# Performance work log

Hardware: AMD Instinct MI355X
Metric: run time of the kernel (lower is better)

Reference implementation:

```python
import jax, jax.numpy as jnp
import numpy as np

N = 100000   # nodes
E = 1600000  # edges (avg degree 16)
D = 128      # input_dim
K = 8        # pe_k
PE = 32      # pe_out_dim
HID = 64     # SignNet hidden
H = 2        # heads
C = 32       # out_channels per head
NEG_SLOPE = 0.2


def setup_inputs() -> dict:
    key = jax.random.key(0)
    ks = jax.random.split(key, 24)
    w = lambda k, shape, s=0.1: jax.random.normal(k, shape, jnp.float32) * s
    return {
        "x": jax.random.normal(ks[0], (N, D), jnp.float32),
        "lap_eigvec": jax.random.normal(ks[1], (N, K), jnp.float32),
        "edge_index": jax.random.randint(ks[2], (2, E), 0, N, jnp.int64),
        # SignNet params: phi (K->HID->HID), rho (HID->PE)
        "phi_w1": w(ks[3], (K, HID)), "phi_b1": jnp.zeros((HID,), jnp.float32),
        "phi_w2": w(ks[4], (HID, HID)), "phi_b2": jnp.zeros((HID,), jnp.float32),
        "rho_w": w(ks[5], (HID, PE)), "rho_b": jnp.zeros((PE,), jnp.float32),
        # GAT layer 0: in = D+PE = 160 -> H*C = 64
        "W0": w(ks[6], (D + PE, H * C)),
        "asrc0": w(ks[7], (H, C)), "adst0": w(ks[8], (H, C)),
        "b0": jnp.zeros((H * C,), jnp.float32),
        # GAT layer 1: in = H*C = 64 -> H*C = 64
        "W1": w(ks[9], (H * C, H * C)),
        "asrc1": w(ks[10], (H, C)), "adst1": w(ks[11], (H, C)),
        "b1": jnp.zeros((H * C,), jnp.float32),
        # final LayerNorm over H*C
        "ln_g": jnp.ones((H * C,), jnp.float32),
        "ln_b": jnp.zeros((H * C,), jnp.float32),
    }


def _gat_layer(x, src, dst, W, a_src, a_dst, b):
    # x: [N, Fin] -> h: [N, H, C]
    h = (x @ W).reshape(x.shape[0], H, C)
    alpha_s = (h * a_src).sum(-1)  # [N, H]
    alpha_d = (h * a_dst).sum(-1)  # [N, H]
    e = jax.nn.leaky_relu(alpha_s[src] + alpha_d[dst], NEG_SLOPE)  # [E, H]
    # softmax over incoming edges per destination node
    e_max = jax.ops.segment_max(e, dst, num_segments=N)  # [N, H]
    e_exp = jnp.exp(e - e_max[dst])
    denom = jax.ops.segment_sum(e_exp, dst, num_segments=N)
    alpha = e_exp / (denom[dst] + 1e-16)  # [E, H]
    msg = h[src] * alpha[:, :, None]      # [E, H, C]
    out = jax.ops.segment_sum(msg, dst, num_segments=N)
    out = out.reshape(x.shape[0], H * C) + b
    return jax.nn.elu(out)


def reference(x, lap_eigvec, edge_index, phi_w1, phi_b1, phi_w2, phi_b2,
              rho_w, rho_b, W0, asrc0, adst0, b0, W1, asrc1, adst1, b1,
              ln_g, ln_b):
    # SignNet: sign-invariant PE  rho(phi(v) + phi(-v))
    def phi(v):
        return jax.nn.relu(jax.nn.relu(v @ phi_w1 + phi_b1) @ phi_w2 + phi_b2)
    pe = (phi(lap_eigvec) + phi(-lap_eigvec)) @ rho_w + rho_b  # [N, PE]
    h = jnp.concatenate([x, pe], axis=-1)  # [N, D+PE]

    src, dst = edge_index[0], edge_index[1]
    h = _gat_layer(h, src, dst, W0, asrc0, adst0, b0)
    h = _gat_layer(h, src, dst, W1, asrc1, adst1, b1)

    # final LayerNorm
    mu = h.mean(-1, keepdims=True)
    var = ((h - mu) ** 2).mean(-1, keepdims=True)
    return (h - mu) * jax.lax.rsqrt(var + 1e-5) * ln_g + ln_b
```

## Files before the change

### kernel.cpp

```cpp
#include <hip/hip_runtime.h>
#include <cstdint>
#include <cstddef>
#include <cstring>

#define TPB 256
#define TILE 8192

typedef float f32x2 __attribute__((ext_vector_type(2)));

__device__ __forceinline__ ushort f2b(float f) {
    union { float f; uint32_t u; } v; v.f = f;
    uint32_t r = (v.u + 0x7FFFu + ((v.u >> 16) & 1u)) >> 16;
    return (ushort)r;
}
__device__ __forceinline__ float b2f(ushort h) {
    union { uint32_t u; float f; } v; v.u = ((uint32_t)h) << 16;
    return v.f;
}
__device__ __forceinline__ float b2f_lo(uint32_t u) {
    union { uint32_t u; float f; } v; v.u = u << 16;
    return v.f;
}
__device__ __forceinline__ float b2f_hi(uint32_t u) {
    union { uint32_t u; float f; } v; v.u = u & 0xFFFF0000u;
    return v.f;
}
__device__ __forceinline__ float f16lo2f(uint32_t u) {
    union { ushort s; _Float16 h; } v; v.s = (ushort)u;
    return (float)v.h;
}
__device__ __forceinline__ uint32_t pack_f16x2(float p0, float p1) {
    auto hp = __builtin_amdgcn_cvt_pkrtz(p0, p1);
    uint32_t pk;
    __builtin_memcpy(&pk, &hp, 4);
    return pk;
}


__global__ __launch_bounds__(TPB) void k_hist(const int* __restrict__ dst, int* __restrict__ hist,
                                              int E, int NB, int NBLK) {
    __shared__ int hc[512];
    const int t = threadIdx.x, blk = blockIdx.x;
    for (int b = t; b < NB; b += TPB) hc[b] = 0;
    __syncthreads();
    const int e0 = blk * TILE;
    for (int i = t; i < TILE; i += TPB) {
        int e = e0 + i;
        if (e < E) atomicAdd(&hc[dst[e] >> 8], 1);
    }
    __syncthreads();
    for (int b = t; b < NB; b += TPB) hist[b * NBLK + blk] = hc[b];
}


__global__ __launch_bounds__(TPB) void k_scan1(const int* __restrict__ a, int* __restrict__ bsum, int total) {
    __shared__ int sh[TPB];
    int base = blockIdx.x * 1024;
    int s = 0;
#pragma unroll
    for (int j = 0; j < 4; ++j) {
        int idx = base + threadIdx.x * 4 + j;
        if (idx < total) s += a[idx];
    }
    sh[threadIdx.x] = s;
    __syncthreads();
    for (int off = 128; off > 0; off >>= 1) {
        if (threadIdx.x < off) sh[threadIdx.x] += sh[threadIdx.x + off];
        __syncthreads();
    }
    if (threadIdx.x == 0) bsum[blockIdx.x] = sh[0];
}

__global__ void k_scan2(int* __restrict__ bsum, int nb) {
    __shared__ int sh[256];
    int t = threadIdx.x;
    int v = (t < nb) ? bsum[t] : 0;
    sh[t] = v;
    __syncthreads();
    for (int off = 1; off < 256; off <<= 1) {
        int u = (t >= off) ? sh[t - off] : 0;
        __syncthreads();
        sh[t] += u;
        __syncthreads();
    }
    if (t < nb) bsum[t] = sh[t] - v;
}

__global__ __launch_bounds__(TPB) void k_scan3(int* __restrict__ a, const int* __restrict__ bsum, int total) {
    __shared__ int sh[TPB];
    int base = blockIdx.x * 1024;
    int v[4];
    int s = 0;
#pragma unroll
    for (int j = 0; j < 4; ++j) {
        int idx = base + threadIdx.x * 4 + j;
        v[j] = (idx < total) ? a[idx] : 0;
        s += v[j];
    }
    sh[threadIdx.x] = s;
    __syncthreads();
    for (int off = 1; off < TPB; off <<= 1) {
        int t = (threadIdx.x >= off) ? sh[threadIdx.x - off] : 0;
        __syncthreads();
        sh[threadIdx.x] += t;
        __syncthreads();
    }
    int pre = bsum[blockIdx.x] + sh[threadIdx.x] - s;
#pragma unroll
    for (int j = 0; j < 4; ++j) {
        int idx = base + threadIdx.x * 4 + j;
        if (idx < total) { a[idx] = pre; pre += v[j]; }
    }
}

__global__ __launch_bounds__(TPB) void k_part(const int* __restrict__ src, const int* __restrict__ dst,
                                              const int* __restrict__ S, int* __restrict__ part,
                                              int E, int NB, int NBLK) {
    __shared__ int hbase[512];
    __shared__ int hcur[512];
    const int t = threadIdx.x, blk = blockIdx.x;
    for (int b = t; b < NB; b += TPB) { hbase[b] = S[b * NBLK + blk]; hcur[b] = 0; }
    __syncthreads();
    const int e0 = blk * TILE;
    for (int i = t; i < TILE; i += TPB) {
        int e = e0 + i;
        if (e < E) {
            int d = dst[e];
            int bu = d >> 8;
            int r = atomicAdd(&hcur[bu], 1);
            part[hbase[bu] + r] = (src[e] << 8) | (d & 255);
        }
    }
}

__global__ __launch_bounds__(TPB) void k_csr(const int* __restrict__ part, const int* __restrict__ S,
                                             int* __restrict__ offs, int* __restrict__ csr,
                                             int E, int N, int NB, int NBLK) {
    __shared__ int cnt[256];
    __shared__ int pre[256];
    const int t = threadIdx.x, b = blockIdx.x;
    const int bstart = S[b * NBLK];
    const int bend = (b + 1 < NB) ? S[(b + 1) * NBLK] : E;
    cnt[t] = 0;
    __syncthreads();
    for (int e = bstart + t; e < bend; e += TPB) atomicAdd(&cnt[part[e] & 255], 1);
    __syncthreads();
    int c = cnt[t];
    pre[t] = c;
    __syncthreads();
    for (int off = 1; off < 256; off <<= 1) {
        int u = (t >= off) ? pre[t - off] : 0;
        __syncthreads();
        pre[t] += u;
        __syncthreads();
    }
    int ex = pre[t] - c;
    int node = b * 256 + t;
    if (node <= N) offs[node] = bstart + ex;
    pre[t] = ex;
    cnt[t] = 0;
    __syncthreads();
    for (int e = bstart + t; e < bend; e += TPB) {
        int pk = part[e];
        int local = pk & 255;
        int r = atomicAdd(&cnt[local], 1);
        csr[bstart + pre[local] + r] = pk >> 8;
    }
}


__global__ __launch_bounds__(TPB) void k_rinit(const float* __restrict__ rho_w, const float* __restrict__ rho_b,
                                               const float* __restrict__ W0, float* __restrict__ R,
                                               float* __restrict__ cvec) {
    const float* Wpe = W0 + 128 * 64;
    int tid = threadIdx.x;
    for (int idx = tid; idx < 64 * 64; idx += TPB) {
        int r = idx >> 6, cc = idx & 63;
        float s = 0.f;
#pragma unroll
        for (int k = 0; k < 32; ++k) s = fmaf(rho_w[r * 32 + k], Wpe[k * 64 + cc], s);
        R[idx] = s;
    }
    if (tid < 64) {
        float s = 0.f;
#pragma unroll
        for (int k = 0; k < 32; ++k) s = fmaf(rho_b[k], Wpe[k * 64 + tid], s);
        cvec[tid] = s;
    }
}


__global__ __launch_bounds__(TPB) void k_sign(const float* __restrict__ eig,
                                              const float* __restrict__ w1, const float* __restrict__ b1,
                                              const float* __restrict__ w2, const float* __restrict__ b2,
                                              ushort* __restrict__ S, int M) {
    __shared__ float eigS[64][9];
    __shared__ float w1s[512];
    __shared__ float b1s[64];
    __shared__ float Ap[64][65];
    __shared__ float Aq[64][65];
    __shared__ float Ws[64][64];
    const int tid = threadIdx.x;
    const int row0 = blockIdx.x * 64;

    for (int i = tid; i < 512; i += TPB) w1s[i] = w1[i];
    if (tid < 64) b1s[tid] = b1[tid];
    for (int i = tid; i < 1024; i += TPB) {
        float4 v = *(const float4*)(w2 + i * 4);
        Ws[0][i * 4 + 0] = v.x; Ws[0][i * 4 + 1] = v.y; Ws[0][i * 4 + 2] = v.z; Ws[0][i * 4 + 3] = v.w;
    }
    {
        int idx = tid * 2;
        int r = idx >> 3, c = idx & 7;
        int row = row0 + r; int rowc = row < M ? row : M - 1;
        float2 v = *(const float2*)(eig + (size_t)rowc * 8 + c);
        eigS[r][c] = v.x; eigS[r][c + 1] = v.y;
    }
    __syncthreads();

    {
        int r = tid >> 2, csub = tid & 3;
        float ev[8];
#pragma unroll
        for (int k = 0; k < 8; ++k) ev[k] = eigS[r][k];
#pragma unroll
        for (int c0 = 0; c0 < 16; ++c0) {
            int c = csub * 16 + c0;
            float t = 0.f;
#pragma unroll
            for (int k = 0; k < 8; ++k) t = fmaf(ev[k], w1s[k * 64 + c], t);
            float bb = b1s[c];
            Ap[c][r] = fmaxf(t + bb, 0.f);
            Aq[c][r] = fmaxf(bb - t, 0.f);
        }
    }
    __syncthreads();

    const int ty = tid >> 4, tx = tid & 15;
    float accp[4][4] = {{0.f}}, accq[4][4] = {{0.f}};
#pragma unroll 8
    for (int kk = 0; kk < 64; ++kk) {
        float ap[4], aq[4], bw[4];
#pragma unroll
        for (int i = 0; i < 4; ++i) { ap[i] = Ap[kk][ty * 4 + i]; aq[i] = Aq[kk][ty * 4 + i]; }
#pragma unroll
        for (int j = 0; j < 4; ++j) bw[j] = Ws[kk][tx * 4 + j];
#pragma unroll
        for (int i = 0; i < 4; ++i)
#pragma unroll
            for (int j = 0; j < 4; ++j) {
                accp[i][j] = fmaf(ap[i], bw[j], accp[i][j]);
                accq[i][j] = fmaf(aq[i], bw[j], accq[i][j]);
            }
    }
#pragma unroll
    for (int i = 0; i < 4; ++i) {
        int row = row0 + ty * 4 + i;
        if (row >= M) continue;
        ushort4 o;
        ushort* op = (ushort*)&o;
#pragma unroll
        for (int j = 0; j < 4; ++j) {
            int col = tx * 4 + j;
            float bb = b2[col];
            float v = fmaxf(accp[i][j] + bb, 0.f) + fmaxf(accq[i][j] + bb, 0.f);
            op[j] = f2b(v);
        }
        *(ushort4*)(S + (size_t)row * 64 + tx * 4) = o;
    }
}


#define BM 64
#define BK 16

__global__ __launch_bounds__(TPB) void k_mm(const float* __restrict__ A1, int K1,
                                            const ushort* __restrict__ A2, int K2,
                                            const float* __restrict__ Wa, const float* __restrict__ Wb,
                                            const float* __restrict__ bias,
                                            const float* __restrict__ a_s, const float* __restrict__ a_d,
                                            float2* __restrict__ as2, float2* __restrict__ ad2,
                                            ushort* __restrict__ out, int M) {
    __shared__ float As[BK][BM + 4];
    __shared__ float Bs[BK][64];
    const int tid = threadIdx.x;
    const int row0 = blockIdx.x * BM;
    const int K = K1 + K2;
    const int ty = tid >> 4, tx = tid & 15;
    float acc[4][4] = {{0.f}};

    for (int k0 = 0; k0 < K; k0 += BK) {
        {
            int r = tid >> 2;
            int cq = (tid & 3) * 4;
            int row = row0 + r;
            int rowc = row < M ? row : M - 1;
            int c = k0 + cq;
            float4 v;
            if (c < K1) {
                v = *(const float4*)(A1 + (size_t)rowc * K1 + c);
            } else {
                const ushort* p = A2 + (size_t)rowc * K2 + (c - K1);
                ushort4 u = *(const ushort4*)p;
                v = make_float4(b2f(u.x), b2f(u.y), b2f(u.z), b2f(u.w));
            }
            As[cq + 0][r] = v.x; As[cq + 1][r] = v.y; As[cq + 2][r] = v.z; As[cq + 3][r] = v.w;
        }
        {
            int rr = tid >> 4;
            int cq2 = (tid & 15) * 4;
            int kk = k0 + rr;
            const float* Wrow = (kk < K1) ? (Wa + (size_t)kk * 64) : (Wb + (size_t)(kk - K1) * 64);
            float4 wv = *(const float4*)(Wrow + cq2);
            Bs[rr][cq2 + 0] = wv.x; Bs[rr][cq2 + 1] = wv.y; Bs[rr][cq2 + 2] = wv.z; Bs[rr][cq2 + 3] = wv.w;
        }
        __syncthreads();
#pragma unroll
        for (int kk = 0; kk < BK; ++kk) {
            float a[4], bw[4];
#pragma unroll
            for (int i = 0; i < 4; ++i) a[i] = As[kk][ty * 4 + i];
#pragma unroll
            for (int j = 0; j < 4; ++j) bw[j] = Bs[kk][tx * 4 + j];
#pragma unroll
            for (int i = 0; i < 4; ++i)
#pragma unroll
                for (int j = 0; j < 4; ++j)
                    acc[i][j] = fmaf(a[i], bw[j], acc[i][j]);
        }
        __syncthreads();
    }

    float s_acc[4] = {0.f, 0.f, 0.f, 0.f}, d_acc[4] = {0.f, 0.f, 0.f, 0.f};
#pragma unroll
    for (int i = 0; i < 4; ++i) {
#pragma unroll
        for (int j = 0; j < 4; ++j) {
            int col = tx * 4 + j;
            float v = acc[i][j];
            if (bias) v += bias[col];
            acc[i][j] = v;
            s_acc[i] = fmaf(v, a_s[col], s_acc[i]);
            d_acc[i] = fmaf(v, a_d[col], d_acc[i]);
        }
    }
#pragma unroll
    for (int m = 1; m <= 4; m <<= 1) {
#pragma unroll
        for (int i = 0; i < 4; ++i) {
            s_acc[i] += __shfl_xor(s_acc[i], m);
            d_acc[i] += __shfl_xor(d_acc[i], m);
        }
    }
    float s_oth[4], d_oth[4];
#pragma unroll
    for (int i = 0; i < 4; ++i) {
        s_oth[i] = __shfl_xor(s_acc[i], 8);
        d_oth[i] = __shfl_xor(d_acc[i], 8);
    }
#pragma unroll
    for (int i = 0; i < 4; ++i) {
        int row = row0 + ty * 4 + i;
        if (row >= M) continue;
        ushort4 o;
        ushort* op = (ushort*)&o;
#pragma unroll
        for (int j = 0; j < 4; ++j) op[j] = f2b(acc[i][j]);
        *(ushort4*)(out + (size_t)row * 64 + tx * 4) = o;
        if (tx == 0) {
            as2[row] = make_float2(s_acc[i], s_oth[i]);
            ad2[row] = make_float2(d_acc[i], d_oth[i]);
        }
    }
}


template <int DO_LN>
__global__ __launch_bounds__(TPB) void k_agg(const int* __restrict__ offs, const int* __restrict__ csr_src,
                                             const ushort* __restrict__ hb,
                                             const float2* __restrict__ as2,
                                             const float2* __restrict__ ad2,
                                             const float* __restrict__ bias,
                                             const float* __restrict__ ln_g,
                                             const float* __restrict__ ln_b,
                                             void* __restrict__ out_v, int M) {
    __shared__ uint2 ep[4][64];
    int w = (blockIdx.x * blockDim.x + threadIdx.x) >> 6;
    int lane = threadIdx.x & 63;
    int wl = threadIdx.x >> 6;
    if (w >= M) return;
    const int sub = lane & 15;
    const int grp = lane >> 4;
    const int c0 = sub * 4;
    const int head = sub >> 3;
    const int hshift = head << 4;

    float2 adv = ad2[w];
    int beg = offs[w], end = offs[w + 1];
    f32x2 acc01 = {0.f, 0.f}, acc23 = {0.f, 0.f};
    float qs = 0.f;

    for (int base = beg; base < end; base += 64) {
        int nk = end - base;
        if (nk > 64) nk = 64;
        int sidx = csr_src[base + (lane < nk ? lane : 0)];
        float2 av = as2[sidx];
        float e0 = av.x + adv.x; e0 = e0 > 0.f ? e0 : 0.2f * e0;
        float e1 = av.y + adv.y; e1 = e1 > 0.f ? e1 : 0.2f * e1;
        float p0 = __expf(e0), p1 = __expf(e1);
        if (lane >= nk) { p0 = 0.f; p1 = 0.f; }
        ep[wl][lane] = make_uint2((uint32_t)sidx, pack_f16x2(p0, p1));

        int j = 0;
        for (; j + 8 <= nk; j += 8) {
            uint2 eA = ep[wl][j + grp];
            uint2 eB = ep[wl][j + 4 + grp];
            uint2 uA = *(const uint2*)(hb + ((uint32_t)eA.x << 6) + c0);
            uint2 uB = *(const uint2*)(hb + ((uint32_t)eB.x << 6) + c0);
            float qA = f16lo2f(eA.y >> hshift);
            float qB = f16lo2f(eB.y >> hshift);
            qs += qA + qB;
            f32x2 hA01 = {b2f_lo(uA.x), b2f_hi(uA.x)};
            f32x2 hA23 = {b2f_lo(uA.y), b2f_hi(uA.y)};
            f32x2 hB01 = {b2f_lo(uB.x), b2f_hi(uB.x)};
            f32x2 hB23 = {b2f_lo(uB.y), b2f_hi(uB.y)};
            acc01 += qA * hA01;
            acc23 += qA * hA23;
            acc01 += qB * hB01;
            acc23 += qB * hB23;
        }
        for (; j < nk; j += 4) {
            int src = j + grp;
            if (src > 63) src = 63;
            uint2 e = ep[wl][src];
            uint2 u = *(const uint2*)(hb + ((uint32_t)e.x << 6) + c0);
            float q = f16lo2f(e.y >> hshift);
            qs += q;
            f32x2 h01 = {b2f_lo(u.x), b2f_hi(u.x)};
            f32x2 h23 = {b2f_lo(u.y), b2f_hi(u.y)};
            acc01 += q * h01;
            acc23 += q * h23;
        }
    }
    float a0 = acc01.x, a1 = acc01.y, a2 = acc23.x, a3 = acc23.y;
    a0 += __shfl_xor(a0, 16); a0 += __shfl_xor(a0, 32);
    a1 += __shfl_xor(a1, 16); a1 += __shfl_xor(a1, 32);
    a2 += __shfl_xor(a2, 16); a2 += __shfl_xor(a2, 32);
    a3 += __shfl_xor(a3, 16); a3 += __shfl_xor(a3, 32);
    qs += __shfl_xor(qs, 16); qs += __shfl_xor(qs, 32);

    float inv = 1.f / (qs + 1e-16f);
    float4 bb = *(const float4*)(bias + c0);
    float o0 = fmaf(a0, inv, bb.x);
    float o1 = fmaf(a1, inv, bb.y);
    float o2 = fmaf(a2, inv, bb.z);
    float o3 = fmaf(a3, inv, bb.w);
    o0 = o0 > 0.f ? o0 : expm1f(o0);
    o1 = o1 > 0.f ? o1 : expm1f(o1);
    o2 = o2 > 0.f ? o2 : expm1f(o2);
    o3 = o3 > 0.f ? o3 : expm1f(o3);

    if (DO_LN) {
        float mu = o0 + o1 + o2 + o3;
#pragma unroll
        for (int m = 1; m <= 8; m <<= 1) mu += __shfl_xor(mu, m);
        mu *= (1.f / 64.f);
        float dv = (o0 - mu) * (o0 - mu) + (o1 - mu) * (o1 - mu)
                 + (o2 - mu) * (o2 - mu) + (o3 - mu) * (o3 - mu);
#pragma unroll
        for (int m = 1; m <= 8; m <<= 1) dv += __shfl_xor(dv, m);
        dv *= (1.f / 64.f);
        float rs = rsqrtf(dv + 1e-5f);
        float4 g = *(const float4*)(ln_g + c0);
        float4 b = *(const float4*)(ln_b + c0);
        o0 = (o0 - mu) * rs * g.x + b.x;
        o1 = (o1 - mu) * rs * g.y + b.y;
        o2 = (o2 - mu) * rs * g.z + b.z;
        o3 = (o3 - mu) * rs * g.w + b.w;
        if (lane < 16) {
            float4* out = (float4*)out_v;
            out[(size_t)w * 16 + sub] = make_float4(o0, o1, o2, o3);
        }
    } else {
        if (lane < 16) {
            uint2 pk2;
            pk2.x = (uint32_t)f2b(o0) | ((uint32_t)f2b(o1) << 16);
            pk2.y = (uint32_t)f2b(o2) | ((uint32_t)f2b(o3) << 16);
            uint2* out = (uint2*)out_v;
            out[(size_t)w * 16 + sub] = pk2;
        }
    }
}


extern "C" void kernel_launch(void* const* d_in, const int* in_sizes, int n_in,
                              void* d_out, int out_size, void* d_ws, size_t ws_size,
                              hipStream_t stream) {
    const float* x      = (const float*)d_in[0];
    const float* eig    = (const float*)d_in[1];
    const int*   ei     = (const int*)d_in[2];
    const float* phi_w1 = (const float*)d_in[3];
    const float* phi_b1 = (const float*)d_in[4];
    const float* phi_w2 = (const float*)d_in[5];
    const float* phi_b2 = (const float*)d_in[6];
    const float* rho_w  = (const float*)d_in[7];
    const float* rho_b  = (const float*)d_in[8];
    const float* W0     = (const float*)d_in[9];
    const float* asrc0  = (const float*)d_in[10];
    const float* adst0  = (const float*)d_in[11];
    const float* b0     = (const float*)d_in[12];
    const float* W1     = (const float*)d_in[13];
    const float* asrc1  = (const float*)d_in[14];
    const float* adst1  = (const float*)d_in[15];
    const float* b1     = (const float*)d_in[16];
    const float* ln_g   = (const float*)d_in[17];
    const float* ln_b   = (const float*)d_in[18];

    const int N = in_sizes[0] / 128;
    const int E = in_sizes[2] / 2;
    const int* esrc = ei;
    const int* edst = ei + E;

    const int NB   = (N >> 8) + 1;
    const int NBLK = (E + TILE - 1) / TILE;

    auto alignup = [](size_t v) { return (v + 255) & ~(size_t)255; };
    char* w = (char*)d_ws;
    int* S      = (int*)w; w += alignup((size_t)NB * NBLK * 4);
    int* bsum   = (int*)w; w += alignup(4096);
    int* part   = (int*)w; w += alignup((size_t)E * 4);
    int* offs   = (int*)w; w += alignup((size_t)(N + 1) * 4);
    int* csr    = (int*)w; w += alignup((size_t)E * 4);
    ushort* Sb  = (ushort*)w; w += alignup((size_t)N * 64 * 2);
    ushort* hb  = (ushort*)w; w += alignup((size_t)N * 64 * 2);
    ushort* g0b = (ushort*)w; w += alignup((size_t)N * 64 * 2);
    float2* as2 = (float2*)w; w += alignup((size_t)N * 8);
    float2* ad2 = (float2*)w; w += alignup((size_t)N * 8);
    float* R    = (float*)w; w += alignup(64 * 64 * 4);
    float* cvec = (float*)w; w += alignup(64 * 4);

    const int tot = NB * NBLK;
    const int nbS = (tot + 1023) / 1024;
    k_hist<<<NBLK, TPB, 0, stream>>>(edst, S, E, NB, NBLK);
    k_scan1<<<nbS, TPB, 0, stream>>>(S, bsum, tot);
    k_scan2<<<1, 256, 0, stream>>>(bsum, nbS);
    k_scan3<<<nbS, TPB, 0, stream>>>(S, bsum, tot);
    k_part<<<NBLK, TPB, 0, stream>>>(esrc, edst, S, part, E, NB, NBLK);
    k_csr<<<NB, TPB, 0, stream>>>(part, S, offs, csr, E, N, NB, NBLK);

    k_rinit<<<1, TPB, 0, stream>>>(rho_w, rho_b, W0, R, cvec);

    int gM = (N + BM - 1) / BM;
    k_sign<<<gM, TPB, 0, stream>>>(eig, phi_w1, phi_b1, phi_w2, phi_b2, Sb, N);

    k_mm<<<gM, TPB, 0, stream>>>(x, 128, Sb, 64, W0, R, cvec, asrc0, adst0, as2, ad2, hb, N);
    int ga = (N + 3) / 4;
    k_agg<0><<<ga, TPB, 0, stream>>>(offs, csr, hb, as2, ad2, b0, nullptr, nullptr, g0b, N);

    k_mm<<<gM, TPB, 0, stream>>>(nullptr, 0, g0b, 64, nullptr, W1, nullptr, asrc1, adst1, as2, ad2, hb, N);
    k_agg<1><<<ga, TPB, 0, stream>>>(offs, csr, hb, as2, ad2, b1, ln_g, ln_b, d_out, N);

    (void)n_in; (void)ws_size; (void)out_size;
}
```

Measured before the change: 282.9 us.

## Replace scalar FP32 GEMM with bf16 MFMA kernel for GAT projections

```diff
diff --git a/kernel.cpp b/kernel.cpp
--- a/kernel.cpp
+++ b/kernel.cpp
@@ -7,6 +7,8 @@
 #define TILE 8192
 
 typedef float f32x2 __attribute__((ext_vector_type(2)));
+typedef float f32x4 __attribute__((ext_vector_type(4)));
+typedef short short8_t __attribute__((ext_vector_type(8)));
 
 __device__ __forceinline__ ushort f2b(float f) {
     union { float f; uint32_t u; } v; v.f = f;
@@ -51,7 +53,6 @@
     __syncthreads();
     for (int b = t; b < NB; b += TPB) hist[b * NBLK + blk] = hc[b];
 }
-
 
 __global__ __launch_bounds__(TPB) void k_scan1(const int* __restrict__ a, int* __restrict__ bsum, int total) {
     __shared__ int sh[TPB];
@@ -271,105 +272,111 @@
 }
 
 
-#define BM 64
-#define BK 16
-
-__global__ __launch_bounds__(TPB) void k_mm(const float* __restrict__ A1, int K1,
-                                            const ushort* __restrict__ A2, int K2,
-                                            const float* __restrict__ Wa, const float* __restrict__ Wb,
-                                            const float* __restrict__ bias,
-                                            const float* __restrict__ a_s, const float* __restrict__ a_d,
-                                            float2* __restrict__ as2, float2* __restrict__ ad2,
-                                            ushort* __restrict__ out, int M) {
-    __shared__ float As[BK][BM + 4];
-    __shared__ float Bs[BK][64];
+template <int K1, int K2>
+__global__ __launch_bounds__(TPB) void k_mmfma(const float* __restrict__ A1,
+                                               const ushort* __restrict__ A2,
+                                               const float* __restrict__ Wa, const float* __restrict__ Wb,
+                                               const float* __restrict__ bias,
+                                               const float* __restrict__ a_s, const float* __restrict__ a_d,
+                                               float2* __restrict__ as2, float2* __restrict__ ad2,
+                                               ushort* __restrict__ out, int M) {
+    constexpr int K = K1 + K2;
+    constexpr int KP = K + 8;
+    __shared__ __align__(16) ushort Ab[64 * KP];
+    __shared__ __align__(16) ushort Wt[64 * KP];
     const int tid = threadIdx.x;
-    const int row0 = blockIdx.x * BM;
-    const int K = K1 + K2;
-    const int ty = tid >> 4, tx = tid & 15;
-    float acc[4][4] = {{0.f}};
-
-    for (int k0 = 0; k0 < K; k0 += BK) {
-        {
-            int r = tid >> 2;
-            int cq = (tid & 3) * 4;
-            int row = row0 + r;
-            int rowc = row < M ? row : M - 1;
-            int c = k0 + cq;
-            float4 v;
-            if (c < K1) {
-                v = *(const float4*)(A1 + (size_t)rowc * K1 + c);
-            } else {
-                const ushort* p = A2 + (size_t)rowc * K2 + (c - K1);
-                ushort4 u = *(const ushort4*)p;
-                v = make_float4(b2f(u.x), b2f(u.y), b2f(u.z), b2f(u.w));
+    const int row0 = blockIdx.x * 64;
+
+    if constexpr (K1 > 0) {
+        for (int idx = tid; idx < 64 * K1 / 4; idx += TPB) {
+            int r = idx / (K1 / 4);
+            int c4 = (idx % (K1 / 4)) * 4;
+            int row = row0 + r; int rowc = row < M ? row : M - 1;
+            float4 v = *(const float4*)(A1 + (size_t)rowc * K1 + c4);
+            Ab[r * KP + c4 + 0] = f2b(v.x);
+            Ab[r * KP + c4 + 1] = f2b(v.y);
+            Ab[r * KP + c4 + 2] = f2b(v.z);
+            Ab[r * KP + c4 + 3] = f2b(v.w);
+        }
+    }
+    if constexpr (K2 > 0) {
+        for (int idx = tid; idx < 64 * K2 / 4; idx += TPB) {
+            int r = idx / (K2 / 4);
+            int c4 = (idx % (K2 / 4)) * 4;
+            int row = row0 + r; int rowc = row < M ? row : M - 1;
+            ushort4 u = *(const ushort4*)(A2 + (size_t)rowc * K2 + c4);
+            Ab[r * KP + K1 + c4 + 0] = u.x;
+            Ab[r * KP + K1 + c4 + 1] = u.y;
+            Ab[r * KP + K1 + c4 + 2] = u.z;
+            Ab[r * KP + K1 + c4 + 3] = u.w;
+        }
+    }
+    for (int idx = tid; idx < K * 16; idx += TPB) {
+        int k = idx / 16;
+        int c4 = (idx % 16) * 4;
+        const float* Wrow = (K1 > 0 && k < K1) ? (Wa + (size_t)k * 64) : (Wb + (size_t)(k - K1) * 64);
+        float4 v = *(const float4*)(Wrow + c4);
+        Wt[(c4 + 0) * KP + k] = f2b(v.x);
+        Wt[(c4 + 1) * KP + k] = f2b(v.y);
+        Wt[(c4 + 2) * KP + k] = f2b(v.z);
+        Wt[(c4 + 3) * KP + k] = f2b(v.w);
+    }
+    __syncthreads();
+
+    const int w = tid >> 6, lane = tid & 63;
+    const int lr = lane & 15, kg = lane >> 4;
+    f32x4 acc0 = {0.f, 0.f, 0.f, 0.f}, acc1 = acc0, acc2 = acc0, acc3 = acc0;
+    const ushort* arow = &Ab[(w * 16 + lr) * KP + kg * 8];
+    const ushort* bp0 = &Wt[(0 + lr) * KP + kg * 8];
+    const ushort* bp1 = &Wt[(16 + lr) * KP + kg * 8];
+    const ushort* bp2 = &Wt[(32 + lr) * KP + kg * 8];
+    const ushort* bp3 = &Wt[(48 + lr) * KP + kg * 8];
+#pragma unroll
+    for (int k0 = 0; k0 < K; k0 += 32) {
+        short8_t af = *(const short8_t*)(arow + k0);
+        short8_t b0 = *(const short8_t*)(bp0 + k0);
+        short8_t b1 = *(const short8_t*)(bp1 + k0);
+        short8_t b2 = *(const short8_t*)(bp2 + k0);
+        short8_t b3 = *(const short8_t*)(bp3 + k0);
+        acc0 = __builtin_amdgcn_mfma_f32_16x16x32_bf16(af, b0, acc0, 0, 0, 0);
+        acc1 = __builtin_amdgcn_mfma_f32_16x16x32_bf16(af, b1, acc1, 0, 0, 0);
+        acc2 = __builtin_amdgcn_mfma_f32_16x16x32_bf16(af, b2, acc2, 0, 0, 0);
+        acc3 = __builtin_amdgcn_mfma_f32_16x16x32_bf16(af, b3, acc3, 0, 0, 0);
+    }
+
+    float asr0 = a_s[lr], asr1 = a_s[16 + lr], asr2 = a_s[32 + lr], asr3 = a_s[48 + lr];
+    float adr0 = a_d[lr], adr1 = a_d[16 + lr], adr2 = a_d[32 + lr], adr3 = a_d[48 + lr];
+    float bb0 = 0.f, bb1 = 0.f, bb2 = 0.f, bb3 = 0.f;
+    if (bias) { bb0 = bias[lr]; bb1 = bias[16 + lr]; bb2 = bias[32 + lr]; bb3 = bias[48 + lr]; }
+
+#pragma unroll
+    for (int i = 0; i < 4; ++i) {
+        int row = row0 + w * 16 + kg * 4 + i;
+        float v0 = acc0[i] + bb0;
+        float v1 = acc1[i] + bb1;
+        float v2 = acc2[i] + bb2;
+        float v3 = acc3[i] + bb3;
+        float sh0 = fmaf(v0, asr0, v1 * asr1);
+        float sh1 = fmaf(v2, asr2, v3 * asr3);
+        float dh0 = fmaf(v0, adr0, v1 * adr1);
+        float dh1 = fmaf(v2, adr2, v3 * adr3);
+#pragma unroll
+        for (int m = 1; m <= 8; m <<= 1) {
+            sh0 += __shfl_xor(sh0, m);
+            sh1 += __shfl_xor(sh1, m);
+            dh0 += __shfl_xor(dh0, m);
+            dh1 += __shfl_xor(dh1, m);
+        }
+        if (row < M) {
+            ushort* orow = out + (size_t)row * 64 + lr;
+            orow[0]  = f2b(v0);
+            orow[16] = f2b(v1);
+            orow[32] = f2b(v2);
+            orow[48] = f2b(v3);
+            if (lr == 0) {
+                as2[row] = make_float2(sh0, sh1);
+                ad2[row] = make_float2(dh0, dh1);
             }
-            As[cq + 0][r] = v.x; As[cq + 1][r] = v.y; As[cq + 2][r] = v.z; As[cq + 3][r] = v.w;
-        }
-        {
-            int rr = tid >> 4;
-            int cq2 = (tid & 15) * 4;
-            int kk = k0 + rr;
-            const float* Wrow = (kk < K1) ? (Wa + (size_t)kk * 64) : (Wb + (size_t)(kk - K1) * 64);
-            float4 wv = *(const float4*)(Wrow + cq2);
-            Bs[rr][cq2 + 0] = wv.x; Bs[rr][cq2 + 1] = wv.y; Bs[rr][cq2 + 2] = wv.z; Bs[rr][cq2 + 3] = wv.w;
-        }
-        __syncthreads();
-#pragma unroll
-        for (int kk = 0; kk < BK; ++kk) {
-            float a[4], bw[4];
-#pragma unroll
-            for (int i = 0; i < 4; ++i) a[i] = As[kk][ty * 4 + i];
-#pragma unroll
-            for (int j = 0; j < 4; ++j) bw[j] = Bs[kk][tx * 4 + j];
-#pragma unroll
-            for (int i = 0; i < 4; ++i)
-#pragma unroll
-                for (int j = 0; j < 4; ++j)
-                    acc[i][j] = fmaf(a[i], bw[j], acc[i][j]);
-        }
-        __syncthreads();
-    }
-
-    float s_acc[4] = {0.f, 0.f, 0.f, 0.f}, d_acc[4] = {0.f, 0.f, 0.f, 0.f};
-#pragma unroll
-    for (int i = 0; i < 4; ++i) {
-#pragma unroll
-        for (int j = 0; j < 4; ++j) {
-            int col = tx * 4 + j;
-            float v = acc[i][j];
-            if (bias) v += bias[col];
-            acc[i][j] = v;
-            s_acc[i] = fmaf(v, a_s[col], s_acc[i]);
-            d_acc[i] = fmaf(v, a_d[col], d_acc[i]);
-        }
-    }
-#pragma unroll
-    for (int m = 1; m <= 4; m <<= 1) {
-#pragma unroll
-        for (int i = 0; i < 4; ++i) {
-            s_acc[i] += __shfl_xor(s_acc[i], m);
-            d_acc[i] += __shfl_xor(d_acc[i], m);
-        }
-    }
-    float s_oth[4], d_oth[4];
-#pragma unroll
-    for (int i = 0; i < 4; ++i) {
-        s_oth[i] = __shfl_xor(s_acc[i], 8);
-        d_oth[i] = __shfl_xor(d_acc[i], 8);
-    }
-#pragma unroll
-    for (int i = 0; i < 4; ++i) {
-        int row = row0 + ty * 4 + i;
-        if (row >= M) continue;
-        ushort4 o;
-        ushort* op = (ushort*)&o;
-#pragma unroll
-        for (int j = 0; j < 4; ++j) op[j] = f2b(acc[i][j]);
-        *(ushort4*)(out + (size_t)row * 64 + tx * 4) = o;
-        if (tx == 0) {
-            as2[row] = make_float2(s_acc[i], s_oth[i]);
-            ad2[row] = make_float2(d_acc[i], d_oth[i]);
         }
     }
 }
@@ -550,14 +557,14 @@
 
     k_rinit<<<1, TPB, 0, stream>>>(rho_w, rho_b, W0, R, cvec);
 
-    int gM = (N + BM - 1) / BM;
+    int gM = (N + 63) / 64;
     k_sign<<<gM, TPB, 0, stream>>>(eig, phi_w1, phi_b1, phi_w2, phi_b2, Sb, N);
 
-    k_mm<<<gM, TPB, 0, stream>>>(x, 128, Sb, 64, W0, R, cvec, asrc0, adst0, as2, ad2, hb, N);
+    k_mmfma<128, 64><<<gM, TPB, 0, stream>>>(x, Sb, W0, R, cvec, asrc0, adst0, as2, ad2, hb, N);
     int ga = (N + 3) / 4;
     k_agg<0><<<ga, TPB, 0, stream>>>(offs, csr, hb, as2, ad2, b0, nullptr, nullptr, g0b, N);
 
-    k_mm<<<gM, TPB, 0, stream>>>(nullptr, 0, g0b, 64, nullptr, W1, nullptr, asrc1, adst1, as2, ad2, hb, N);
+    k_mmfma<0, 64><<<gM, TPB, 0, stream>>>(nullptr, g0b, nullptr, W1, nullptr, asrc1, adst1, as2, ad2, hb, N);
     k_agg<1><<<ga, TPB, 0, stream>>>(offs, csr, hb, as2, ad2, b1, ln_g, ln_b, d_out, N);
 
     (void)n_in; (void)ws_size; (void)out_size;
```

Measured after the change: 263.2 us. 1.07x faster.
